# Optimization experiments

Measured on AMD Instinct MI355X. Metric: run time of the kernel, lower is better.

Reference implementation:

```python
import jax, jax.numpy as jnp
import numpy as np

N = 50000          # nodes
E = 1_600_000      # edges (avg degree 32)
F_IN = 128         # input node features
G = 64             # graphs in batch
LAYERS = [(F_IN, 4, 16), (64, 4, 16), (64, 4, 16), (64, 1, 64)]  # (in, heads, ch)


def setup_inputs() -> dict:
    key = jax.random.key(0)
    ks = iter(jax.random.split(key, 32))
    inp = {
        "x": jax.random.normal(next(ks), (N, F_IN), dtype=jnp.float32),
        "edge_index": jax.random.randint(next(ks), (2, E), 0, N, dtype=jnp.int64),
        "batch": jnp.sort(jax.random.randint(next(ks), (N,), 0, G, dtype=jnp.int64)),
    }
    for i, (fi, h, c) in enumerate(LAYERS, 1):
        inp[f"W{i}"] = jax.random.normal(next(ks), (fi, h * c), dtype=jnp.float32) / np.sqrt(fi)
        inp[f"as{i}"] = jax.random.normal(next(ks), (h, c), dtype=jnp.float32) / np.sqrt(c)
        inp[f"ad{i}"] = jax.random.normal(next(ks), (h, c), dtype=jnp.float32) / np.sqrt(c)
        inp[f"b{i}"] = jnp.zeros((h * c,), dtype=jnp.float32)
    return inp


def _segment_softmax(logits, seg, num_segments):
    # logits: [E, H], softmax per destination node, per head
    m = jax.ops.segment_max(logits, seg, num_segments=num_segments)
    ex = jnp.exp(logits - m[seg])
    s = jax.ops.segment_sum(ex, seg, num_segments=num_segments)
    return ex / (s[seg] + 1e-16)


def _gat_conv(x, src, dst, W, a_src, a_dst, b, heads, ch):
    n = x.shape[0]
    h = (x @ W).reshape(n, heads, ch)                      # [N, H, C]
    alpha_s = jnp.einsum('nhc,hc->nh', h, a_src)           # [N, H]
    alpha_d = jnp.einsum('nhc,hc->nh', h, a_dst)           # [N, H]
    e = jax.nn.leaky_relu(alpha_s[src] + alpha_d[dst], 0.2)  # [E, H]
    alpha = _segment_softmax(e, dst, n)                    # [E, H]
    msg = h[src] * alpha[:, :, None]                       # [E, H, C]
    out = jax.ops.segment_sum(msg, dst, num_segments=n)    # [N, H, C]
    return out.reshape(n, heads * ch) + b


def reference(x, edge_index, batch,
              W1, as1, ad1, b1, W2, as2, ad2, b2,
              W3, as3, ad3, b3, W4, as4, ad4, b4):
    # PyG GATConv add_self_loops=True
    loop = jnp.arange(N, dtype=edge_index.dtype)
    src = jnp.concatenate([edge_index[0], loop])
    dst = jnp.concatenate([edge_index[1], loop])

    params = [(W1, as1, ad1, b1), (W2, as2, ad2, b2), (W3, as3, ad3, b3), (W4, as4, ad4, b4)]
    h = x
    for (W, a_s, a_d, b), (_, heads, ch) in zip(params, LAYERS):
        h = jax.nn.leaky_relu(_gat_conv(h, src, dst, W, a_s, a_d, b, heads, ch), 0.01)

    # global mean pool over batch assignment
    sums = jax.ops.segment_sum(h, batch, num_segments=G)                    # [G, 64]
    cnts = jax.ops.segment_sum(jnp.ones((N,), h.dtype), batch, num_segments=G)
    return sums / jnp.maximum(cnts, 1.0)[:, None]
```

## Files before the change

### kernel.cpp

```cpp
#include <hip/hip_runtime.h>


#define MAXDEG 96
#define NGRAPH 64
#define NB 2048
#define ALS_BOUND 16.0f

__device__ __forceinline__ unsigned short f2bf(float f) {
  unsigned int u = __float_as_uint(f);
  u += 0x7fffu + ((u >> 16) & 1u);
  return (unsigned short)(u >> 16);
}
__device__ __forceinline__ float lrelu2(float v) { return (v > 0.f) ? v : 0.2f * v; }


__global__ __launch_bounds__(256) void k_build(const int* __restrict__ ei,
                                               const int* __restrict__ batch,
                                               int* __restrict__ cursor,
                                               int* __restrict__ gstart,
                                               unsigned short* __restrict__ ell,
                                               int E, int N) {
  int tid = blockIdx.x * blockDim.x + threadIdx.x;
  int nthr = gridDim.x * blockDim.x;
  for (int n = tid; n < N; n += nthr) {
    int b = batch[n];
    if (n == 0) {
      for (int g = 0; g <= b; ++g) gstart[g] = 0;
    } else {
      int pb = batch[n - 1];
      if (b != pb)
        for (int g = pb + 1; g <= b; ++g) gstart[g] = n;
    }
    if (n == N - 1) {
      for (int g = b + 1; g <= NGRAPH; ++g) gstart[g] = N;
    }
  }
  int w = blockIdx.x & 7;
  int bg = blockIdx.x >> 3;
  int range = (N + 7) / 8;
  int lo = w * range;
  int hi = lo + range; if (hi > N) hi = N;
  int t = bg * blockDim.x + threadIdx.x;
  int stride = (gridDim.x >> 3) * blockDim.x;
  for (int e = t; e < E; e += stride) {
    int dst = ei[E + e];
    if (dst >= lo && dst < hi) {
      int slot = atomicAdd(&cursor[dst], 1);
      if (slot < MAXDEG) ell[(size_t)dst * MAXDEG + slot] = (unsigned short)ei[e];
    }
  }
}


template <int K, int H>
__global__ __launch_bounds__(256) void k_T(
    const float* __restrict__ xin, const float* __restrict__ W,
    const float* __restrict__ avs, const float* __restrict__ avd,
    unsigned short* __restrict__ hbuf, float* __restrict__ als,
    float* __restrict__ ald, int N) {
  constexpr int C = 64 / H;
  int lane = threadIdx.x & 63;
  int wid = (blockIdx.x * blockDim.x + threadIdx.x) >> 6;
  if (wid >= N) return;
  float sA = avs[lane], sD = avd[lane];
  const float* xr = xin + (size_t)wid * K;
  float r0 = xr[lane];
  float r1 = (K == 128) ? xr[64 + lane] : 0.f;
  float acc = 0.f;
#pragma unroll
  for (int k = 0; k < K; ++k) {
    float xk = __shfl((k < 64) ? r0 : r1, k & 63, 64);
    acc += xk * W[k * 64 + lane];
  }
  hbuf[(size_t)wid * 64 + lane] = f2bf(acc);
  float ps = acc * sA, pd = acc * sD;
#pragma unroll
  for (int off = 1; off < C; off <<= 1) {
    ps += __shfl_xor(ps, off, 64);
    pd += __shfl_xor(pd, off, 64);
  }
  if ((lane & (C - 1)) == 0) {
    als[wid * H + lane / C] = ps;
    ald[wid * H + lane / C] = pd;
  }
}


template <int H>
__global__ __launch_bounds__(256) void k_A(
    const int* __restrict__ deg, const unsigned short* __restrict__ ell,
    const float* __restrict__ als, const float* __restrict__ ald,
    const unsigned short* __restrict__ hbuf, const float* __restrict__ bias,
    float* __restrict__ feat, int N) {
  constexpr int C = 64 / H;
  int lane = threadIdx.x & 63;
  int wid = (blockIdx.x * blockDim.x + threadIdx.x) >> 6;
  if (wid >= N) return;
  int j = lane & 7;
  int g = lane >> 3;
  int hf = (8 * j) / C;
  int d = deg[wid];
  if (d > MAXDEG) d = MAXDEG;
  const unsigned short* row = ell + (size_t)wid * MAXDEG;
  float aa = ald[wid * H + hf];
  float ash = als[wid * H + hf];
  float mm = lrelu2(ALS_BOUND + aa);
  float a0 = 0.f, a1 = 0.f, a2 = 0.f, a3 = 0.f;
  float a4 = 0.f, a5 = 0.f, a6 = 0.f, a7 = 0.f, sw = 0.f;
  for (int i = 0; i < d; i += 8) {
    uint4 iv = *(const uint4*)(row + i);
    unsigned int word = ((g >> 1) == 0) ? iv.x : ((g >> 1) == 1) ? iv.y
                        : ((g >> 1) == 2) ? iv.z : iv.w;
    int s = (g & 1) ? (int)(word >> 16) : (int)(word & 0xffffu);
    bool valid = (i + g) < d;
    s = valid ? s : wid;
    float v = lrelu2(als[s * H + hf] + aa);
    float wgt = valid ? __expf(v - mm) : 0.f;
    uint4 hv = *(const uint4*)(hbuf + (size_t)s * 64 + j * 8);
    sw += wgt;
    a0 += wgt * __uint_as_float(hv.x << 16);
    a1 += wgt * __uint_as_float(hv.x & 0xffff0000u);
    a2 += wgt * __uint_as_float(hv.y << 16);
    a3 += wgt * __uint_as_float(hv.y & 0xffff0000u);
    a4 += wgt * __uint_as_float(hv.z << 16);
    a5 += wgt * __uint_as_float(hv.z & 0xffff0000u);
    a6 += wgt * __uint_as_float(hv.w << 16);
    a7 += wgt * __uint_as_float(hv.w & 0xffff0000u);
  }
#pragma unroll
  for (int off = 8; off < 64; off <<= 1) {
    sw += __shfl_xor(sw, off, 64);
    a0 += __shfl_xor(a0, off, 64);
    a1 += __shfl_xor(a1, off, 64);
    a2 += __shfl_xor(a2, off, 64);
    a3 += __shfl_xor(a3, off, 64);
    a4 += __shfl_xor(a4, off, 64);
    a5 += __shfl_xor(a5, off, 64);
    a6 += __shfl_xor(a6, off, 64);
    a7 += __shfl_xor(a7, off, 64);
  }
  {
    float v = lrelu2(ash + aa);
    float wgt = __expf(v - mm);
    uint4 hv = *(const uint4*)(hbuf + (size_t)wid * 64 + j * 8);
    sw += wgt;
    a0 += wgt * __uint_as_float(hv.x << 16);
    a1 += wgt * __uint_as_float(hv.x & 0xffff0000u);
    a2 += wgt * __uint_as_float(hv.y << 16);
    a3 += wgt * __uint_as_float(hv.y & 0xffff0000u);
    a4 += wgt * __uint_as_float(hv.z << 16);
    a5 += wgt * __uint_as_float(hv.z & 0xffff0000u);
    a6 += wgt * __uint_as_float(hv.w << 16);
    a7 += wgt * __uint_as_float(hv.w & 0xffff0000u);
  }
  float inv = 1.f / (sw + 1e-16f);
  if (g == 0) {
    const float4 bv = *(const float4*)(bias + j * 8);
    float4 o;
    o.x = a0 * inv + bv.x; o.x = (o.x > 0.f) ? o.x : 0.01f * o.x;
    o.y = a1 * inv + bv.y; o.y = (o.y > 0.f) ? o.y : 0.01f * o.y;
    o.z = a2 * inv + bv.z; o.z = (o.z > 0.f) ? o.z : 0.01f * o.z;
    o.w = a3 * inv + bv.w; o.w = (o.w > 0.f) ? o.w : 0.01f * o.w;
    *(float4*)(feat + (size_t)wid * 64 + j * 8) = o;
  } else if (g == 1) {
    const float4 bv = *(const float4*)(bias + j * 8 + 4);
    float4 o;
    o.x = a4 * inv + bv.x; o.x = (o.x > 0.f) ? o.x : 0.01f * o.x;
    o.y = a5 * inv + bv.y; o.y = (o.y > 0.f) ? o.y : 0.01f * o.y;
    o.z = a6 * inv + bv.z; o.z = (o.z > 0.f) ? o.z : 0.01f * o.z;
    o.w = a7 * inv + bv.w; o.w = (o.w > 0.f) ? o.w : 0.01f * o.w;
    *(float4*)(feat + (size_t)wid * 64 + j * 8 + 4) = o;
  }
}


__global__ __launch_bounds__(256) void k_pool(const int* __restrict__ gstart,
                                              const float* __restrict__ feat,
                                              float* __restrict__ out) {
  __shared__ float psum[256];
  int g = blockIdx.x, t = threadIdx.x, f = t & 63, r = t >> 6;
  int s = gstart[g], e = gstart[g + 1];
  float acc = 0.f;
  for (int n = s + r; n < e; n += 4) acc += feat[(size_t)n * 64 + f];
  psum[t] = acc;
  __syncthreads();
  if (r == 0) {
    float tot = psum[f] + psum[64 + f] + psum[128 + f] + psum[192 + f];
    out[g * 64 + f] = tot / fmaxf((float)(e - s), 1.0f);
  }
}


extern "C" void kernel_launch(void* const* d_in, const int* in_sizes, int n_in,
                              void* d_out, int out_size, void* d_ws, size_t ws_size,
                              hipStream_t stream) {
  const float* x = (const float*)d_in[0];
  const int* ei = (const int*)d_in[1];
  const int* batch = (const int*)d_in[2];
  const float* W1 = (const float*)d_in[3];
  const float* as1 = (const float*)d_in[4];
  const float* ad1 = (const float*)d_in[5];
  const float* b1 = (const float*)d_in[6];
  const float* W2 = (const float*)d_in[7];
  const float* as2 = (const float*)d_in[8];
  const float* ad2 = (const float*)d_in[9];
  const float* b2 = (const float*)d_in[10];
  const float* W3 = (const float*)d_in[11];
  const float* as3 = (const float*)d_in[12];
  const float* ad3 = (const float*)d_in[13];
  const float* b3 = (const float*)d_in[14];
  const float* W4 = (const float*)d_in[15];
  const float* as4 = (const float*)d_in[16];
  const float* ad4 = (const float*)d_in[17];
  const float* b4 = (const float*)d_in[18];
  float* out = (float*)d_out;

  const int N = in_sizes[2];
  const int E = in_sizes[1] / 2;

  size_t off = 0;
  auto carve = [&](size_t bytes) {
    void* q = (char*)d_ws + off;
    off = (off + bytes + 255) & ~(size_t)255;
    return q;
  };
  int* cursor = (int*)carve((size_t)N * 4);
  int* gstart = (int*)carve((size_t)(NGRAPH + 1) * 4);
  unsigned short* ell = (unsigned short*)carve((size_t)N * MAXDEG * 2);
  unsigned short* hbuf = (unsigned short*)carve((size_t)N * 64 * 2);
  float* als = (float*)carve((size_t)N * 4 * 4);
  float* ald = (float*)carve((size_t)N * 4 * 4);
  float* feat = (float*)carve((size_t)N * 64 * 4);
  (void)ws_size;

  int wb = (N + 3) / 4;

  hipMemsetAsync(cursor, 0, (size_t)N * 4, stream);
  k_build<<<NB, 256, 0, stream>>>(ei, batch, cursor, gstart, ell, E, N);

  k_T<128, 4><<<wb, 256, 0, stream>>>(x, W1, as1, ad1, hbuf, als, ald, N);
  k_A<4><<<wb, 256, 0, stream>>>(cursor, ell, als, ald, hbuf, b1, feat, N);
  k_T<64, 4><<<wb, 256, 0, stream>>>(feat, W2, as2, ad2, hbuf, als, ald, N);
  k_A<4><<<wb, 256, 0, stream>>>(cursor, ell, als, ald, hbuf, b2, feat, N);
  k_T<64, 4><<<wb, 256, 0, stream>>>(feat, W3, as3, ad3, hbuf, als, ald, N);
  k_A<4><<<wb, 256, 0, stream>>>(cursor, ell, als, ald, hbuf, b3, feat, N);
  k_T<64, 1><<<wb, 256, 0, stream>>>(feat, W4, as4, ad4, hbuf, als, ald, N);
  k_A<1><<<wb, 256, 0, stream>>>(cursor, ell, als, ald, hbuf, b4, feat, N);

  k_pool<<<NGRAPH, 256, 0, stream>>>(gstart, feat, out);
}
```

Before: 617.4 us.

## Keep weight column in registers and loop waves persistently over nodes in k_T

The feature-transform kernel now launches a fixed grid of waves, each looping over many nodes. Each lane loads its weight column into registers once, instead of re-reading W from cache for every node. Node rows are read through a wave-uniform (readfirstlane) address so they can come in as scalar loads, replacing the per-k shuffle broadcast. For the 128-wide first layer, weights are packed as bf16 pairs to fit in registers, which adds rounding error on W1 and raises register pressure.

```diff
diff --git a/kernel.cpp b/kernel.cpp
--- a/kernel.cpp
+++ b/kernel.cpp
@@ -4,6 +4,7 @@
 #define MAXDEG 96
 #define NGRAPH 64
 #define NB 2048
+#define TB 1024
 #define ALS_BOUND 16.0f
 
 __device__ __forceinline__ unsigned short f2bf(float f) {
@@ -60,28 +61,51 @@
     float* __restrict__ ald, int N) {
   constexpr int C = 64 / H;
   int lane = threadIdx.x & 63;
-  int wid = (blockIdx.x * blockDim.x + threadIdx.x) >> 6;
-  if (wid >= N) return;
+  int wave0 = (blockIdx.x * blockDim.x + threadIdx.x) >> 6;
+  int nw = (gridDim.x * blockDim.x) >> 6;
   float sA = avs[lane], sD = avd[lane];
-  const float* xr = xin + (size_t)wid * K;
-  float r0 = xr[lane];
-  float r1 = (K == 128) ? xr[64 + lane] : 0.f;
-  float acc = 0.f;
-#pragma unroll
-  for (int k = 0; k < K; ++k) {
-    float xk = __shfl((k < 64) ? r0 : r1, k & 63, 64);
-    acc += xk * W[k * 64 + lane];
-  }
-  hbuf[(size_t)wid * 64 + lane] = f2bf(acc);
-  float ps = acc * sA, pd = acc * sD;
-#pragma unroll
-  for (int off = 1; off < C; off <<= 1) {
-    ps += __shfl_xor(ps, off, 64);
-    pd += __shfl_xor(pd, off, 64);
-  }
-  if ((lane & (C - 1)) == 0) {
-    als[wid * H + lane / C] = ps;
-    ald[wid * H + lane / C] = pd;
+
+  float wf[K == 64 ? 64 : 1];
+  unsigned int wp[K == 128 ? 64 : 1];
+  if constexpr (K == 64) {
+#pragma unroll
+    for (int k = 0; k < 64; ++k) wf[k] = W[k * 64 + lane];
+  } else {
+#pragma unroll
+    for (int kk = 0; kk < 64; ++kk) {
+      float w0 = W[(2 * kk) * 64 + lane];
+      float w1 = W[(2 * kk + 1) * 64 + lane];
+      wp[kk] = ((unsigned)f2bf(w0)) | (((unsigned)f2bf(w1)) << 16);
+    }
+  }
+
+  for (int wid = wave0; wid < N; wid += nw) {
+    unsigned int boff =
+        __builtin_amdgcn_readfirstlane((unsigned int)(wid * (K * 4)));
+    const float* xr = (const float*)((const char*)xin + boff);
+    float acc = 0.f;
+    if constexpr (K == 64) {
+#pragma unroll
+      for (int k = 0; k < 64; ++k) acc += xr[k] * wf[k];
+    } else {
+#pragma unroll
+      for (int kk = 0; kk < 64; ++kk) {
+        unsigned int w = wp[kk];
+        acc += xr[2 * kk] * __uint_as_float(w << 16);
+        acc += xr[2 * kk + 1] * __uint_as_float(w & 0xffff0000u);
+      }
+    }
+    hbuf[(size_t)wid * 64 + lane] = f2bf(acc);
+    float ps = acc * sA, pd = acc * sD;
+#pragma unroll
+    for (int off = 1; off < C; off <<= 1) {
+      ps += __shfl_xor(ps, off, 64);
+      pd += __shfl_xor(pd, off, 64);
+    }
+    if ((lane & (C - 1)) == 0) {
+      als[wid * H + lane / C] = ps;
+      ald[wid * H + lane / C] = pd;
+    }
   }
 }
 
@@ -238,13 +262,13 @@
   hipMemsetAsync(cursor, 0, (size_t)N * 4, stream);
   k_build<<<NB, 256, 0, stream>>>(ei, batch, cursor, gstart, ell, E, N);
 
-  k_T<128, 4><<<wb, 256, 0, stream>>>(x, W1, as1, ad1, hbuf, als, ald, N);
+  k_T<128, 4><<<TB, 256, 0, stream>>>(x, W1, as1, ad1, hbuf, als, ald, N);
   k_A<4><<<wb, 256, 0, stream>>>(cursor, ell, als, ald, hbuf, b1, feat, N);
-  k_T<64, 4><<<wb, 256, 0, stream>>>(feat, W2, as2, ad2, hbuf, als, ald, N);
+  k_T<64, 4><<<TB, 256, 0, stream>>>(feat, W2, as2, ad2, hbuf, als, ald, N);
   k_A<4><<<wb, 256, 0, stream>>>(cursor, ell, als, ald, hbuf, b2, feat, N);
-  k_T<64, 4><<<wb, 256, 0, stream>>>(feat, W3, as3, ad3, hbuf, als, ald, N);
+  k_T<64, 4><<<TB, 256, 0, stream>>>(feat, W3, as3, ad3, hbuf, als, ald, N);
   k_A<4><<<wb, 256, 0, stream>>>(cursor, ell, als, ald, hbuf, b3, feat, N);
-  k_T<64, 1><<<wb, 256, 0, stream>>>(feat, W4, as4, ad4, hbuf, als, ald, N);
+  k_T<64, 1><<<TB, 256, 0, stream>>>(feat, W4, as4, ad4, hbuf, als, ald, N);
   k_A<1><<<wb, 256, 0, stream>>>(cursor, ell, als, ald, hbuf, b4, feat, N);
 
   k_pool<<<NGRAPH, 256, 0, stream>>>(gstart, feat, out);
```

Result: faster. 529.6 us (-14.2%).
